# Kernel optimization log

Hardware: AMD Instinct MI355X
Metric: run time of the kernel (lower is better)

## Reference

```python
import jax, jax.numpy as jnp
import numpy as np

N_SAMPLES = 8192
N_EDGES = 4096
INPUT_DIM = 512
DK = 64
OUTPUT_DIM = 256


def setup_inputs() -> dict:
    key = jax.random.key(0)
    k1, k2, k3, k4, k5, k6 = jax.random.split(key, 6)

    def xavier(k, shape):
        bound = np.sqrt(6.0 / (shape[0] + shape[1])).astype(np.float32)
        return jax.random.uniform(k, shape, jnp.float32, -bound, bound)

    X = jax.random.normal(k1, (N_SAMPLES, INPUT_DIM), jnp.float32)
    Y = jax.random.normal(k2, (N_EDGES, INPUT_DIM), jnp.float32)
    H = jax.random.randint(k3, (N_SAMPLES, N_EDGES), 0, 2, jnp.int32)
    W_q = xavier(k4, (INPUT_DIM, DK))
    W_k = xavier(k5, (INPUT_DIM, DK))
    W_v = xavier(k6, (INPUT_DIM, OUTPUT_DIM))
    return {"X": X, "Y": Y, "H": H, "W_q": W_q, "W_k": W_k, "W_v": W_v}


def reference(X, Y, H, W_q, W_k, W_v):
    # Q: (n_edges, dk), K: (n_samples, dk)
    Q = Y @ W_q
    K = X @ W_k
    scale = jnp.sqrt(jnp.asarray(K.shape[1], jnp.float32))
    # scores: (n_edges, n_samples), masked by hypergraph incidence H.T
    scores = (Q @ K.T) / scale
    scores = jnp.where(H.T == 0, -jnp.inf, scores)
    attn = jax.nn.softmax(scores, axis=-1)
    # attention-weighted vertex features projected by W_v
    return attn @ (X @ W_v)
```

## Files before the change

kernel.cpp:

```cpp
#include <hip/hip_runtime.h>
#include <hip/hip_bf16.h>

#define NS 8192
#define NE 4096
#define DIN 512
#define DK 64
#define DV 256
#define NCHUNK 8
#define CHUNK (NS / NCHUNK)
#define NTILE (CHUNK / 64)

typedef __attribute__((ext_vector_type(8))) short bf16x8;
typedef __attribute__((ext_vector_type(4))) float f32x4;
typedef __attribute__((ext_vector_type(8))) unsigned short ushort8;
typedef __attribute__((ext_vector_type(4))) unsigned short ushort4v;

#define L2E 1.44269504088896f

__device__ __forceinline__ unsigned short f2bf(float f) {
    union { float f; unsigned int u; } v; v.f = f;
    unsigned int u = v.u;
    unsigned int r = u + 0x7fffu + ((u >> 16) & 1u);
    return (unsigned short)(r >> 16);
}

union ProjSmem {
    struct { unsigned short As[64][40]; unsigned short Bst[64][40]; } s;
    unsigned short Ct[64][72];
};

__global__ __launch_bounds__(256, 4) void proj_kernel(
    const float* __restrict__ X, const float* __restrict__ Y,
    const float* __restrict__ Wq, const float* __restrict__ Wk,
    const float* __restrict__ Wv,
    unsigned short* __restrict__ Qb, unsigned short* __restrict__ Kb,
    unsigned short* __restrict__ Vt) {

    int b = blockIdx.x;
    const float* A; const float* B; unsigned short* out;
    int N, m0, n0; float scale; bool tr;
    if (b < 64)       { A = Y; B = Wq; out = Qb; N = 64;  m0 = b * 64;        n0 = 0;            scale = 0.125f * L2E; tr = false; }
    else if (b < 192) { A = X; B = Wk; out = Kb; N = 64;  m0 = (b - 64) * 64; n0 = 0;            scale = 1.0f;         tr = false; }
    else              { int bb = b - 192;
                        A = X; B = Wv; out = Vt; N = 256; m0 = (bb >> 2) * 64; n0 = (bb & 3) * 64; scale = 1.0f;       tr = true; }

    __shared__ ProjSmem sm;
    int tid = threadIdx.x;
    int lane = tid & 63, w = tid >> 6;
    int c = lane & 15, g = lane >> 4;
    int wr = w >> 1, wc = w & 1;

    f32x4 acc[2][2] = {};

    for (int kt = 0; kt < 16; ++kt) {
        int k0 = kt * 32;
        __syncthreads();
        #pragma unroll
        for (int it = 0; it < 2; ++it) {
            int idx = it * 256 + tid;
            {
                int r = idx >> 3, c4 = (idx & 7) * 4;
                float4 v = *(const float4*)&A[(size_t)(m0 + r) * DIN + k0 + c4];
                ushort4v t; t.x = f2bf(v.x); t.y = f2bf(v.y); t.z = f2bf(v.z); t.w = f2bf(v.w);
                *(ushort4v*)&sm.s.As[r][c4] = t;
            }
            {
                int kk = idx >> 4, c4 = (idx & 15) * 4;
                float4 v = *(const float4*)&B[(size_t)(k0 + kk) * N + n0 + c4];
                sm.s.Bst[c4 + 0][kk] = f2bf(v.x);
                sm.s.Bst[c4 + 1][kk] = f2bf(v.y);
                sm.s.Bst[c4 + 2][kk] = f2bf(v.z);
                sm.s.Bst[c4 + 3][kk] = f2bf(v.w);
            }
        }
        __syncthreads();

        bf16x8 af[2], bfr[2];
        #pragma unroll
        for (int fr = 0; fr < 2; ++fr)
            af[fr] = *(const bf16x8*)&sm.s.As[wr * 32 + fr * 16 + c][8 * g];
        #pragma unroll
        for (int fc = 0; fc < 2; ++fc)
            bfr[fc] = *(const bf16x8*)&sm.s.Bst[wc * 32 + fc * 16 + c][8 * g];
        #pragma unroll
        for (int fr = 0; fr < 2; ++fr)
            #pragma unroll
            for (int fc = 0; fc < 2; ++fc)
                acc[fr][fc] = __builtin_amdgcn_mfma_f32_16x16x32_bf16(af[fr], bfr[fc], acc[fr][fc], 0, 0, 0);
    }

    if (!tr) {
        #pragma unroll
        for (int fr = 0; fr < 2; ++fr)
            #pragma unroll
            for (int fc = 0; fc < 2; ++fc)
                #pragma unroll
                for (int i = 0; i < 4; ++i) {
                    int row = wr * 32 + fr * 16 + 4 * g + i;
                    int col = wc * 32 + fc * 16 + c;
                    out[(size_t)(m0 + row) * N + n0 + col] = f2bf(acc[fr][fc][i] * scale);
                }
    } else {
        __syncthreads();
        #pragma unroll
        for (int fr = 0; fr < 2; ++fr)
            #pragma unroll
            for (int fc = 0; fc < 2; ++fc)
                #pragma unroll
                for (int i = 0; i < 4; ++i) {
                    int row = wr * 32 + fr * 16 + 4 * g + i;
                    int col = wc * 32 + fc * 16 + c;
                    sm.Ct[col][row] = f2bf(acc[fr][fc][i]);
                }
        __syncthreads();
        int nl = tid >> 2, q = tid & 3;
        #pragma unroll
        for (int gg = 0; gg < 2; ++gg) {
            int G = q * 2 + gg;
            int ks = G >> 2, gq = G & 3;
            union { ushort4v h[2]; ushort8 v8; } u;
            u.h[0] = *(const ushort4v*)&sm.Ct[nl][ks * 32 + gq * 4];
            u.h[1] = *(const ushort4v*)&sm.Ct[nl][ks * 32 + 16 + gq * 4];
            *(ushort8*)&out[(size_t)(n0 + nl) * NS + m0 + G * 8] = u.v8;
        }
    }
}

__global__ __launch_bounds__(256, 2) void flash_kernel(
    const unsigned short* __restrict__ Qb, const unsigned short* __restrict__ Kb,
    const unsigned short* __restrict__ Vt, const int* __restrict__ H,
    unsigned int* __restrict__ pacc, float* __restrict__ pm, float* __restrict__ pl) {

    int bid = blockIdx.x;
    int ch = bid & 7, eb = bid >> 3;
    int e0 = eb * 64;
    int sbeg = ch * CHUNK;

    __shared__ unsigned short Ks[64 * 64];
    __shared__ unsigned short Vts[256 * 64];

    int tid = threadIdx.x, lane = tid & 63, w = tid >> 6;
    int c = lane & 15, g = lane >> 4;
    int eW = e0 + w * 16 + c;
    int cc = tid & 7;

    bf16x8 qf[2];
    #pragma unroll
    for (int ks = 0; ks < 2; ++ks)
        qf[ks] = *(const bf16x8*)&Qb[(size_t)eW * DK + ks * 32 + 8 * g];

    f32x4 o[16] = {};
    float m = -1e30f, l = 0.0f;

    #pragma unroll 1
    for (int t = 0; t < NTILE; ++t) {
        int s0 = sbeg + t * 64;

        __syncthreads();

        #pragma unroll
        for (int it = 0; it < 2; ++it) {
            int idx = it * 256 + tid;
            int r = idx >> 3;
            int cs = cc ^ (r & 7);
            __builtin_amdgcn_global_load_lds(
                (const void*)&Kb[(size_t)(s0 + r) * DK + cs * 8],
                (void*)((char*)Ks + (it * 256 + w * 64) * 16), 16, 0, 0);
        }
        #pragma unroll
        for (int it = 0; it < 8; ++it) {
            int idx = it * 256 + tid;
            int v = idx >> 3;
            int cs = cc ^ (v & 7);
            __builtin_amdgcn_global_load_lds(
                (const void*)&Vt[(size_t)v * NS + s0 + cs * 8],
                (void*)((char*)Vts + (it * 256 + w * 64) * 16), 16, 0, 0);
        }

        int hv[16];
        #pragma unroll
        for (int fr = 0; fr < 4; ++fr)
            #pragma unroll
            for (int i = 0; i < 4; ++i)
                hv[fr * 4 + i] = H[(size_t)(s0 + fr * 16 + 4 * g + i) * NE + eW];

        __syncthreads();

        f32x4 st[4] = {};
        #pragma unroll
        for (int ks = 0; ks < 2; ++ks)
            #pragma unroll
            for (int fr = 0; fr < 4; ++fr) {
                int u = ((fr * 16 + c) * 64 + ks * 32 + 8 * g) ^ ((c & 7) << 3);
                bf16x8 a = *(const bf16x8*)&Ks[u];
                st[fr] = __builtin_amdgcn_mfma_f32_16x16x32_bf16(a, qf[ks], st[fr], 0, 0, 0);
            }

        float pmax = -1e30f;
        #pragma unroll
        for (int fr = 0; fr < 4; ++fr)
            #pragma unroll
            for (int i = 0; i < 4; ++i) {
                float sv = hv[fr * 4 + i] ? st[fr][i] : -1e30f;
                st[fr][i] = sv;
                pmax = fmaxf(pmax, sv);
            }
        pmax = fmaxf(pmax, __shfl_xor(pmax, 16));
        pmax = fmaxf(pmax, __shfl_xor(pmax, 32));

        if (!__all(pmax <= m + 8.0f)) {
            float mn = fmaxf(m, pmax);
            float al = exp2f(m - mn);
            l *= al;
            #pragma unroll
            for (int vb = 0; vb < 16; ++vb) o[vb] *= al;
            m = mn;
        }

        float lp = 0.0f;
        #pragma unroll
        for (int fr = 0; fr < 4; ++fr)
            #pragma unroll
            for (int i = 0; i < 4; ++i) {
                float e = exp2f(st[fr][i] - m);
                st[fr][i] = e;
                lp += e;
            }
        lp += __shfl_xor(lp, 16);
        lp += __shfl_xor(lp, 32);
        l += lp;

        unsigned int pk[8];
        #pragma unroll
        for (int fr = 0; fr < 4; ++fr)
            #pragma unroll
            for (int hf = 0; hf < 2; ++hf) {
                union { __hip_bfloat162 h; unsigned int u; } cv;
                cv.h = __float22bfloat162_rn(make_float2(st[fr][2 * hf], st[fr][2 * hf + 1]));
                pk[fr * 2 + hf] = cv.u;
            }

        #pragma unroll
        for (int ks = 0; ks < 2; ++ks) {
            union { unsigned int u[4]; bf16x8 s; } bb;
            bb.u[0] = pk[4 * ks]; bb.u[1] = pk[4 * ks + 1];
            bb.u[2] = pk[4 * ks + 2]; bb.u[3] = pk[4 * ks + 3];
            #pragma unroll
            for (int vb = 0; vb < 16; ++vb) {
                int u = ((vb * 16 + c) * 64 + ks * 32 + 8 * g) ^ ((c & 7) << 3);
                bf16x8 av = *(const bf16x8*)&Vts[u];
                o[vb] = __builtin_amdgcn_mfma_f32_16x16x32_bf16(av, bb.s, o[vb], 0, 0, 0);
            }
        }
    }

    size_t base = (size_t)ch * (DV / 2) * NE;
    #pragma unroll
    for (int vb = 0; vb < 16; ++vb)
        #pragma unroll
        for (int ip = 0; ip < 2; ++ip) {
            union { __hip_bfloat162 h; unsigned int u; } cv;
            cv.h = __float22bfloat162_rn(make_float2(o[vb][2 * ip], o[vb][2 * ip + 1]));
            pacc[base + (size_t)(vb * 8 + 2 * g + ip) * NE + eW] = cv.u;
        }
    if (g == 0) {
        pm[ch * NE + eW] = m;
        pl[ch * NE + eW] = l;
    }
}

__global__ __launch_bounds__(256, 4) void combine_kernel(
    const unsigned int* __restrict__ pacc, const float* __restrict__ pm,
    const float* __restrict__ pl, float* __restrict__ out) {

    __shared__ float T[64][68];
    int bid = blockIdx.x;
    int eb = bid & 63, vb = bid >> 6;
    int e0 = eb * 64, v0 = vb * 64;
    int tid = threadIdx.x;
    int el = tid & 63, vh = tid >> 6;
    int e = e0 + el;

    float mv[NCHUNK]; float M = -1e30f;
    #pragma unroll
    for (int chn = 0; chn < NCHUNK; ++chn) {
        mv[chn] = pm[chn * NE + e];
        M = fmaxf(M, mv[chn]);
    }
    float den = 0.0f; float wch[NCHUNK];
    #pragma unroll
    for (int chn = 0; chn < NCHUNK; ++chn) {
        wch[chn] = exp2f(mv[chn] - M);
        den += wch[chn] * pl[chn * NE + e];
    }
    float rden = 1.0f / den;

    #pragma unroll
    for (int kp = 0; kp < 8; ++kp) {
        int vp = vb * 32 + vh * 8 + kp;
        float n0 = 0.0f, n1 = 0.0f;
        #pragma unroll
        for (int chn = 0; chn < NCHUNK; ++chn) {
            unsigned int pk = pacc[((size_t)chn * (DV / 2) + vp) * NE + e];
            n0 += wch[chn] * __uint_as_float(pk << 16);
            n1 += wch[chn] * __uint_as_float(pk & 0xffff0000u);
        }
        T[el][(vh * 8 + kp) * 2]     = n0 * rden;
        T[el][(vh * 8 + kp) * 2 + 1] = n1 * rden;
    }
    __syncthreads();

    int er = tid >> 2, c16 = (tid & 3) * 16;
    #pragma unroll
    for (int j = 0; j < 4; ++j) {
        float4 vv = *(const float4*)&T[er][c16 + 4 * j];
        *(float4*)&out[(size_t)(e0 + er) * DV + v0 + c16 + 4 * j] = vv;
    }
}

#define QB_OFF   ((size_t)0)
#define KB_OFF   (QB_OFF + (size_t)NE * DK * 2)
#define VT_OFF   (KB_OFF + (size_t)NS * DK * 2)
#define PACC_OFF (VT_OFF + (size_t)DV * NS * 2)
#define PM_OFF   (PACC_OFF + (size_t)NCHUNK * (DV / 2) * NE * 4)
#define PL_OFF   (PM_OFF + (size_t)NCHUNK * NE * 4)

extern "C" void kernel_launch(void* const* d_in, const int* in_sizes, int n_in,
                              void* d_out, int out_size, void* d_ws, size_t ws_size,
                              hipStream_t stream) {
    const float* X  = (const float*)d_in[0];
    const float* Y  = (const float*)d_in[1];
    const int*   H  = (const int*)d_in[2];
    const float* Wq = (const float*)d_in[3];
    const float* Wk = (const float*)d_in[4];
    const float* Wv = (const float*)d_in[5];

    char* ws = (char*)d_ws;
    unsigned short* Qb = (unsigned short*)(ws + QB_OFF);
    unsigned short* Kb = (unsigned short*)(ws + KB_OFF);
    unsigned short* Vt = (unsigned short*)(ws + VT_OFF);
    unsigned int* pacc = (unsigned int*)(ws + PACC_OFF);
    float* pm   = (float*)(ws + PM_OFF);
    float* pl   = (float*)(ws + PL_OFF);

    proj_kernel<<<704, 256, 0, stream>>>(X, Y, Wq, Wk, Wv, Qb, Kb, Vt);
    flash_kernel<<<512, 256, 0, stream>>>(Qb, Kb, Vt, H, pacc, pm, pl);
    combine_kernel<<<256, 256, 0, stream>>>(pacc, pm, pl, (float*)d_out);
}
```

Before: 80.19 us.

## Double-buffer K/V tiles in LDS and prefetch next tile during compute

```diff
diff --git a/kernel.cpp b/kernel.cpp
--- a/kernel.cpp
+++ b/kernel.cpp
@@ -126,6 +126,27 @@
     }
 }
 
+__device__ __forceinline__ void stage_kv(
+    const unsigned short* __restrict__ Kb, const unsigned short* __restrict__ Vt,
+    unsigned short* bufp, int s0, int tid, int w, int cc) {
+    #pragma unroll
+    for (int it = 0; it < 2; ++it) {
+        int r = (it * 256 + tid) >> 3;
+        int cs = cc ^ (r & 7);
+        __builtin_amdgcn_global_load_lds(
+            (const void*)&Kb[(size_t)(s0 + r) * DK + cs * 8],
+            (void*)((char*)bufp + (it * 256 + w * 64) * 16), 16, 0, 0);
+    }
+    #pragma unroll
+    for (int it = 0; it < 8; ++it) {
+        int v = (it * 256 + tid) >> 3;
+        int cs = cc ^ (v & 7);
+        __builtin_amdgcn_global_load_lds(
+            (const void*)&Vt[(size_t)v * NS + s0 + cs * 8],
+            (void*)((char*)bufp + 8192 + (it * 256 + w * 64) * 16), 16, 0, 0);
+    }
+}
+
 __global__ __launch_bounds__(256, 2) void flash_kernel(
     const unsigned short* __restrict__ Qb, const unsigned short* __restrict__ Kb,
     const unsigned short* __restrict__ Vt, const int* __restrict__ H,
@@ -136,13 +157,13 @@
     int e0 = eb * 64;
     int sbeg = ch * CHUNK;
 
-    __shared__ unsigned short Ks[64 * 64];
-    __shared__ unsigned short Vts[256 * 64];
+    __shared__ unsigned short smem[2][20480];
 
     int tid = threadIdx.x, lane = tid & 63, w = tid >> 6;
     int c = lane & 15, g = lane >> 4;
     int eW = e0 + w * 16 + c;
     int cc = tid & 7;
+    int swz = (c & 7) << 3;
 
     bf16x8 qf[2];
     #pragma unroll
@@ -151,50 +172,37 @@
 
     f32x4 o[16] = {};
     float m = -1e30f, l = 0.0f;
+
+    stage_kv(Kb, Vt, smem[0], sbeg, tid, w, cc);
+    __syncthreads();
 
     #pragma unroll 1
     for (int t = 0; t < NTILE; ++t) {
         int s0 = sbeg + t * 64;
-
-        __syncthreads();
-
-        #pragma unroll
-        for (int it = 0; it < 2; ++it) {
-            int idx = it * 256 + tid;
-            int r = idx >> 3;
-            int cs = cc ^ (r & 7);
-            __builtin_amdgcn_global_load_lds(
-                (const void*)&Kb[(size_t)(s0 + r) * DK + cs * 8],
-                (void*)((char*)Ks + (it * 256 + w * 64) * 16), 16, 0, 0);
-        }
-        #pragma unroll
-        for (int it = 0; it < 8; ++it) {
-            int idx = it * 256 + tid;
-            int v = idx >> 3;
-            int cs = cc ^ (v & 7);
-            __builtin_amdgcn_global_load_lds(
-                (const void*)&Vt[(size_t)v * NS + s0 + cs * 8],
-                (void*)((char*)Vts + (it * 256 + w * 64) * 16), 16, 0, 0);
-        }
-
+        const unsigned short* bufp = smem[t & 1];
+
+        const int* Hp = H + (size_t)s0 * NE + eW;
         int hv[16];
         #pragma unroll
         for (int fr = 0; fr < 4; ++fr)
             #pragma unroll
             for (int i = 0; i < 4; ++i)
-                hv[fr * 4 + i] = H[(size_t)(s0 + fr * 16 + 4 * g + i) * NE + eW];
-
-        __syncthreads();
-
+                hv[fr * 4 + i] = Hp[(size_t)(fr * 16 + 4 * g + i) * NE];
+
+        if (t + 1 < NTILE)
+            stage_kv(Kb, Vt, smem[(t + 1) & 1], s0 + 64, tid, w, cc);
+
+        __builtin_amdgcn_s_setprio(1);
         f32x4 st[4] = {};
         #pragma unroll
         for (int ks = 0; ks < 2; ++ks)
             #pragma unroll
             for (int fr = 0; fr < 4; ++fr) {
-                int u = ((fr * 16 + c) * 64 + ks * 32 + 8 * g) ^ ((c & 7) << 3);
-                bf16x8 a = *(const bf16x8*)&Ks[u];
+                int u = ((fr * 16 + c) * 64 + ks * 32 + 8 * g) ^ swz;
+                bf16x8 a = *(const bf16x8*)&bufp[u];
                 st[fr] = __builtin_amdgcn_mfma_f32_16x16x32_bf16(a, qf[ks], st[fr], 0, 0, 0);
             }
+        __builtin_amdgcn_s_setprio(0);
 
         float pmax = -1e30f;
         #pragma unroll
@@ -240,6 +248,7 @@
                 pk[fr * 2 + hf] = cv.u;
             }
 
+        __builtin_amdgcn_s_setprio(1);
         #pragma unroll
         for (int ks = 0; ks < 2; ++ks) {
             union { unsigned int u[4]; bf16x8 s; } bb;
@@ -247,11 +256,14 @@
             bb.u[2] = pk[4 * ks + 2]; bb.u[3] = pk[4 * ks + 3];
             #pragma unroll
             for (int vb = 0; vb < 16; ++vb) {
-                int u = ((vb * 16 + c) * 64 + ks * 32 + 8 * g) ^ ((c & 7) << 3);
-                bf16x8 av = *(const bf16x8*)&Vts[u];
+                int u = 4096 + (((vb * 16 + c) * 64 + ks * 32 + 8 * g) ^ swz);
+                bf16x8 av = *(const bf16x8*)&bufp[u];
                 o[vb] = __builtin_amdgcn_mfma_f32_16x16x32_bf16(av, bb.s, o[vb], 0, 0, 0);
             }
         }
+        __builtin_amdgcn_s_setprio(0);
+
+        __syncthreads();
     }
 
     size_t base = (size_t)ch * (DV / 2) * NE;
```

Result: slower. 85.86 us (+7.1%).
